# Kernel optimization log

Hardware: AMD Instinct MI355X
Metric: run time of the kernel (lower is better)

## Reference

```python
import jax, jax.numpy as jnp
import numpy as np

NOISE = 0.01
AUTOINVERT = True

def setup_inputs() -> dict:
    key = jax.random.key(0)
    a = jax.random.uniform(key, (64, 3, 768, 768), dtype=jnp.float32)
    return {"a": a}

def reference(a) -> jnp.ndarray:
    # [B,C,H,W] -> channel mean -> [B,1,H,W]
    g = jnp.mean(a, axis=1, keepdims=True)
    # per-image min subtraction
    mn = jnp.min(g, axis=(1, 2, 3), keepdims=True)
    g = g - mn
    # per-image divide by max(0.5, max)
    mx = jnp.maximum(jnp.float32(0.5), jnp.max(g, axis=(1, 2, 3), keepdims=True))
    g = g / mx
    # autoinvert when mean brightness > 0.5
    if AUTOINVERT:
        mean = jnp.mean(g, axis=(1, 2, 3), keepdims=True)
        g = jnp.where(mean > 0.5, 1.0 - g, g)
    # additive gaussian noise (fixed key for determinism)
    if NOISE > 0:
        noise = NOISE * jax.random.normal(jax.random.key(1), g.shape, g.dtype)
        g = g + noise
    return jnp.clip(g, 0.0, 1.0)
```

## Files before the change

kernel.cpp:

```cpp
#include <hip/hip_runtime.h>
#include <stdint.h>

#define BATCH 64
#define PIX   589824
#define PIX4  147456
#define IMG3  442368
#define N_TOT 37748736
#define N4    9437184
#define BPI   144
#define NPART (BATCH*BPI)

typedef float f32x4 __attribute__((ext_vector_type(4)));

__device__ f32x4  g_gray4[N4];
__device__ float  g_pmin[NPART];
__device__ float  g_pmax[NPART];
__device__ float  g_psum[NPART];
__device__ float2 g_stats[BATCH];

__device__ __forceinline__ uint32_t rotl32(uint32_t x, int r) {
    return (x << r) | (x >> (32 - r));
}

__device__ __forceinline__ void threefry01(uint32_t x0, uint32_t x1,
                                           uint32_t& o0, uint32_t& o1) {
    const uint32_t ks0 = 0u, ks1 = 1u, ks2 = 0x1BD11BDBu;
    x0 += ks0; x1 += ks1;
#define RND(r) { x0 += x1; x1 = rotl32(x1, (r)); x1 ^= x0; }
    RND(13) RND(15) RND(26) RND(6)   x0 += ks1; x1 += ks2 + 1u;
    RND(17) RND(29) RND(16) RND(24)  x0 += ks2; x1 += ks0 + 2u;
    RND(13) RND(15) RND(26) RND(6)   x0 += ks0; x1 += ks1 + 3u;
    RND(17) RND(29) RND(16) RND(24)  x0 += ks1; x1 += ks2 + 4u;
    RND(13) RND(15) RND(26) RND(6)   x0 += ks2; x1 += ks0 + 5u;
#undef RND
    o0 = x0; o1 = x1;
}

__device__ __forceinline__ uint32_t jax_bits32(uint32_t i) {
    uint32_t w0, w1;
    threefry01(0u, i, w0, w1);
    return w0 ^ w1;
}

__device__ __forceinline__ float noise_from_bits(uint32_t bits) {
    float f = __uint_as_float((bits >> 9) | 0x3f800000u) - 1.0f;
    const float LO = __uint_as_float(0xBF7FFFFFu);
    float u = fmaxf(LO, fmaf(f, 2.0f, LO));
    float w  = -log1pf(-u * u);
    float ws = w - 2.5f;
    float wb = sqrtf(w) - 3.0f;
    float p1 = 2.81022636e-08f;
    p1 = fmaf(p1, ws, 3.43273939e-07f);
    p1 = fmaf(p1, ws, -3.5233877e-06f);
    p1 = fmaf(p1, ws, -4.39150654e-06f);
    p1 = fmaf(p1, ws, 0.00021858087f);
    p1 = fmaf(p1, ws, -0.00125372503f);
    p1 = fmaf(p1, ws, -0.00417768164f);
    p1 = fmaf(p1, ws, 0.246640727f);
    p1 = fmaf(p1, ws, 1.50140941f);
    float p2 = -0.000200214257f;
    p2 = fmaf(p2, wb, 0.000100950558f);
    p2 = fmaf(p2, wb, 0.00134934322f);
    p2 = fmaf(p2, wb, -0.00367342844f);
    p2 = fmaf(p2, wb, 0.00573950773f);
    p2 = fmaf(p2, wb, -0.0076224613f);
    p2 = fmaf(p2, wb, 0.00943887047f);
    p2 = fmaf(p2, wb, 1.00167406f);
    p2 = fmaf(p2, wb, 2.83297682f);
    float p = (w < 5.0f) ? p1 : p2;
    return 0.01f * 1.41421354f * (p * u);
}

__global__ __launch_bounds__(256) void k1_reduce(const float* __restrict__ a) {
    const int b = blockIdx.y;
    const int tid = threadIdx.x;
    const f32x4* a4 = (const f32x4*)a;
    const int base = b * IMG3;
    const int chunk = blockIdx.x * (256 * 4);
    const float inv3 = 1.0f / 3.0f;
    float mn = 1e30f, mx = -1e30f, sm = 0.0f;
#pragma unroll
    for (int j = 0; j < 4; ++j) {
        int p4 = chunk + j * 256 + tid;
        f32x4 c0 = __builtin_nontemporal_load(&a4[base + p4]);
        f32x4 c1 = __builtin_nontemporal_load(&a4[base + PIX4 + p4]);
        f32x4 c2 = __builtin_nontemporal_load(&a4[base + 2 * PIX4 + p4]);
        f32x4 g = (c0 + c1 + c2) * inv3;
        g_gray4[b * PIX4 + p4] = g;
        mn = fminf(mn, fminf(fminf(g.x, g.y), fminf(g.z, g.w)));
        mx = fmaxf(mx, fmaxf(fmaxf(g.x, g.y), fmaxf(g.z, g.w)));
        sm += (g.x + g.y) + (g.z + g.w);
    }
#pragma unroll
    for (int off = 32; off; off >>= 1) {
        mn = fminf(mn, __shfl_down(mn, off));
        mx = fmaxf(mx, __shfl_down(mx, off));
        sm += __shfl_down(sm, off);
    }
    __shared__ float smn[4], smx[4], ssm[4];
    int wave = tid >> 6, lane = tid & 63;
    if (lane == 0) { smn[wave] = mn; smx[wave] = mx; ssm[wave] = sm; }
    __syncthreads();
    if (tid == 0) {
        mn = fminf(fminf(smn[0], smn[1]), fminf(smn[2], smn[3]));
        mx = fmaxf(fmaxf(smx[0], smx[1]), fmaxf(smx[2], smx[3]));
        sm = (ssm[0] + ssm[1]) + (ssm[2] + ssm[3]);
        int pi = b * BPI + blockIdx.x;
        g_pmin[pi] = mn; g_pmax[pi] = mx; g_psum[pi] = sm;
    }
}

__global__ __launch_bounds__(64) void k2_finalize() {
    const int b = blockIdx.x;
    const int t = threadIdx.x;
    float mn = 1e30f, mx = -1e30f;
    double sm = 0.0;
    for (int k = t; k < BPI; k += 64) {
        mn = fminf(mn, g_pmin[b * BPI + k]);
        mx = fmaxf(mx, g_pmax[b * BPI + k]);
        sm += (double)g_psum[b * BPI + k];
    }
#pragma unroll
    for (int off = 32; off; off >>= 1) {
        mn = fminf(mn, __shfl_down(mn, off));
        mx = fmaxf(mx, __shfl_down(mx, off));
        sm += __shfl_down(sm, off);
    }
    if (t == 0) {
        float div = fmaxf(0.5f, mx - mn);
        float mean_norm = (float)((sm / (double)PIX - (double)mn) / (double)div);
        float s, tt;
        if (mean_norm > 0.5f) { s = -1.0f / div; tt = 1.0f + mn / div; }
        else                  { s =  1.0f / div; tt = -mn / div; }
        g_stats[b] = make_float2(s, tt);
    }
}

__global__ __launch_bounds__(256) void k3_apply(float* __restrict__ out) {
    const int gt0 = blockIdx.x * 256 + threadIdx.x;
    const int b0 = gt0 / PIX4;
    const int b  = (BATCH - 1) - b0;
    const int gt = b * PIX4 + (gt0 - b0 * PIX4);
    const float2 st = g_stats[b];

    f32x4 g = g_gray4[gt];

    const uint32_t i = (uint32_t)gt * 4u;
    float n0 = noise_from_bits(jax_bits32(i + 0u));
    float n1 = noise_from_bits(jax_bits32(i + 1u));
    float n2 = noise_from_bits(jax_bits32(i + 2u));
    float n3 = noise_from_bits(jax_bits32(i + 3u));

    f32x4 o;
    o.x = fminf(fmaxf(fmaf(st.x, g.x, st.y) + n0, 0.0f), 1.0f);
    o.y = fminf(fmaxf(fmaf(st.x, g.y, st.y) + n1, 0.0f), 1.0f);
    o.z = fminf(fmaxf(fmaf(st.x, g.z, st.y) + n2, 0.0f), 1.0f);
    o.w = fminf(fmaxf(fmaf(st.x, g.w, st.y) + n3, 0.0f), 1.0f);

    __builtin_nontemporal_store(o, &((f32x4*)out)[gt]);
}

extern "C" void kernel_launch(void* const* d_in, const int* in_sizes, int n_in,
                              void* d_out, int out_size, void* d_ws, size_t ws_size,
                              hipStream_t stream) {
    const float* a = (const float*)d_in[0];
    float* out = (float*)d_out;
    (void)d_ws; (void)ws_size;

    k1_reduce<<<dim3(BPI, BATCH), 256, 0, stream>>>(a);
    k2_finalize<<<BATCH, 64, 0, stream>>>();
    k3_apply<<<N4 / 256, 256, 0, stream>>>(out);
}
```

Before: 779.0 us.

## Drop gray intermediate buffer and re-read input in phases of sixteen images

Stops writing the grayscale intermediate to global memory. The apply kernel now recomputes the channel mean from the original input. Processing runs in four phases of 16 images, so each phase's input (about 113 MB) can stay resident in the large last-level cache between the reduce pass and the apply pass. Nontemporal loads are replaced with normal loads to allow that caching, at the cost of twelve launches instead of three and less parallelism per launch.

```diff
diff --git a/kernel.cpp b/kernel.cpp
--- a/kernel.cpp
+++ b/kernel.cpp
@@ -1,5 +1,6 @@
 #include <hip/hip_runtime.h>
 #include <stdint.h>
+
 
 #define BATCH 64
 #define PIX   589824
@@ -9,10 +10,11 @@
 #define N4    9437184
 #define BPI   144
 #define NPART (BATCH*BPI)
+#define IPP   16
+#define NPHASE 4
 
 typedef float f32x4 __attribute__((ext_vector_type(4)));
 
-__device__ f32x4  g_gray4[N4];
 __device__ float  g_pmin[NPART];
 __device__ float  g_pmax[NPART];
 __device__ float  g_psum[NPART];
@@ -71,8 +73,9 @@
     return 0.01f * 1.41421354f * (p * u);
 }
 
-__global__ __launch_bounds__(256) void k1_reduce(const float* __restrict__ a) {
-    const int b = blockIdx.y;
+__global__ __launch_bounds__(256) void k1_reduce(const float* __restrict__ a,
+                                                 int img0) {
+    const int b = img0 + blockIdx.y;
     const int tid = threadIdx.x;
     const f32x4* a4 = (const f32x4*)a;
     const int base = b * IMG3;
@@ -82,11 +85,10 @@
 #pragma unroll
     for (int j = 0; j < 4; ++j) {
         int p4 = chunk + j * 256 + tid;
-        f32x4 c0 = __builtin_nontemporal_load(&a4[base + p4]);
-        f32x4 c1 = __builtin_nontemporal_load(&a4[base + PIX4 + p4]);
-        f32x4 c2 = __builtin_nontemporal_load(&a4[base + 2 * PIX4 + p4]);
+        f32x4 c0 = a4[base + p4];
+        f32x4 c1 = a4[base + PIX4 + p4];
+        f32x4 c2 = a4[base + 2 * PIX4 + p4];
         f32x4 g = (c0 + c1 + c2) * inv3;
-        g_gray4[b * PIX4 + p4] = g;
         mn = fminf(mn, fminf(fminf(g.x, g.y), fminf(g.z, g.w)));
         mx = fmaxf(mx, fmaxf(fmaxf(g.x, g.y), fmaxf(g.z, g.w)));
         sm += (g.x + g.y) + (g.z + g.w);
@@ -110,8 +112,8 @@
     }
 }
 
-__global__ __launch_bounds__(64) void k2_finalize() {
-    const int b = blockIdx.x;
+__global__ __launch_bounds__(64) void k2_finalize(int img0) {
+    const int b = img0 + blockIdx.x;
     const int t = threadIdx.x;
     float mn = 1e30f, mx = -1e30f;
     double sm = 0.0;
@@ -136,14 +138,23 @@
     }
 }
 
-__global__ __launch_bounds__(256) void k3_apply(float* __restrict__ out) {
-    const int gt0 = blockIdx.x * 256 + threadIdx.x;
-    const int b0 = gt0 / PIX4;
-    const int b  = (BATCH - 1) - b0;
-    const int gt = b * PIX4 + (gt0 - b0 * PIX4);
+__global__ __launch_bounds__(256) void k3_apply(const float* __restrict__ a,
+                                                float* __restrict__ out,
+                                                int img0) {
+    const int lt = blockIdx.x * 256 + threadIdx.x;
+    const int bl = lt / PIX4;
+    const int b  = img0 + bl;
+    const int pf = lt - bl * PIX4;
+    const int gt = b * PIX4 + pf;
     const float2 st = g_stats[b];
 
-    f32x4 g = g_gray4[gt];
+    const f32x4* a4 = (const f32x4*)a;
+    const int ab = b * IMG3;
+    const float inv3 = 1.0f / 3.0f;
+    f32x4 c0 = a4[ab + pf];
+    f32x4 c1 = a4[ab + PIX4 + pf];
+    f32x4 c2 = a4[ab + 2 * PIX4 + pf];
+    f32x4 g = (c0 + c1 + c2) * inv3;
 
     const uint32_t i = (uint32_t)gt * 4u;
     float n0 = noise_from_bits(jax_bits32(i + 0u));
@@ -167,7 +178,10 @@
     float* out = (float*)d_out;
     (void)d_ws; (void)ws_size;
 
-    k1_reduce<<<dim3(BPI, BATCH), 256, 0, stream>>>(a);
-    k2_finalize<<<BATCH, 64, 0, stream>>>();
-    k3_apply<<<N4 / 256, 256, 0, stream>>>(out);
+    for (int p = 0; p < NPHASE; ++p) {
+        const int img0 = p * IPP;
+        k1_reduce<<<dim3(BPI, IPP), 256, 0, stream>>>(a, img0);
+        k2_finalize<<<IPP, 64, 0, stream>>>(img0);
+        k3_apply<<<(IPP * PIX4) / 256, 256, 0, stream>>>(a, out, img0);
+    }
 }
```

After: 813.8 us. 1.04x slower.
